# Kernel tuning notes

Measured on AMD Instinct MI355X. Metric: run time of the kernel, lower is better.

## Reference

```python
import jax, jax.numpy as jnp
import numpy as np

B, C, H, W = 64, 256, 64, 64
RATIO, K = 16, 8
PLANES = C // 2          # context_modeling hidden = int(in_planes*0.5)
HIDDEN = C // RATIO      # net hidden
ATT_CH = K // 2          # kernel-attention hidden
TEMP = 30.0
EPS = 1e-5


def setup_inputs() -> dict:
    key = jax.random.key(0)
    ks = jax.random.split(key, 16)
    s = lambda k, shape: jax.random.normal(k, shape, dtype=jnp.float32) * 0.05
    return {
        "x": jax.random.normal(ks[0], (B, C, H, W), dtype=jnp.float32),
        # conv_mask: Conv2d(C,1,1) with bias
        "w_mask": s(ks[1], (1, C)), "b_mask": jnp.zeros((1,), jnp.float32),
        # context_modeling: Conv2d(C,PLANES,1)+bias, LayerNorm([PLANES,1,1]), GELU, Conv2d(PLANES,C,1)+bias
        "w_cm1": s(ks[2], (PLANES, C)), "b_cm1": jnp.zeros((PLANES,), jnp.float32),
        "ln_w": jnp.ones((PLANES,), jnp.float32), "ln_b": jnp.zeros((PLANES,), jnp.float32),
        "w_cm2": s(ks[3], (C, PLANES)), "b_cm2": jnp.zeros((C,), jnp.float32),
        # net: Conv2d(C,HIDDEN,1,bias=False), ReLU, Conv2d(HIDDEN,K,1,bias=False)
        "w_net1": s(ks[4], (HIDDEN, C)), "w_net2": s(ks[5], (K, HIDDEN)),
        # kernel attention branch (K != 1)
        "w_fc": s(ks[6], (ATT_CH, K)),
        "bn_w": jnp.ones((ATT_CH,), jnp.float32), "bn_b": jnp.zeros((ATT_CH,), jnp.float32),
        "bn_mean": jnp.zeros((ATT_CH,), jnp.float32), "bn_var": jnp.ones((ATT_CH,), jnp.float32),
        "w_kfc": s(ks[7], (K, ATT_CH)),
    }


def reference(x, w_mask, b_mask, w_cm1, b_cm1, ln_w, ln_b, w_cm2, b_cm2,
              w_net1, w_net2, w_fc, bn_w, bn_b, bn_mean, bn_var, w_kfc):
    b, c, h, w = x.shape
    # beta_c: global average pool -> [B, C]
    beta_c = jnp.mean(x, axis=(2, 3))
    # global_pool: softmax(conv_mask(x)) over HW, spatially weighted sum of x
    mask = jnp.einsum('bchw,oc->bohw', x, w_mask)[:, 0] + b_mask[0]      # [B,H,W]
    mask = jax.nn.softmax(mask.reshape(b, h * w), axis=-1)               # softmax over HW
    context = jnp.einsum('bchw,bs->bc', x, mask.reshape(b, h, w).reshape(b, -1).reshape(b, h * w)) if False else \
        jnp.einsum('bcs,bs->bc', x.reshape(b, c, h * w), mask)           # [B,C]
    # context_modeling: 1x1 conv -> LayerNorm over channels -> GELU -> 1x1 conv
    t = context @ w_cm1.T + b_cm1                                        # [B, PLANES]
    mu = jnp.mean(t, axis=-1, keepdims=True)
    var = jnp.mean((t - mu) ** 2, axis=-1, keepdims=True)
    t = (t - mu) * jax.lax.rsqrt(var + EPS) * ln_w + ln_b
    t = jax.nn.gelu(t, approximate=False)
    beta_g = t @ w_cm2.T + b_cm2                                         # [B, C]
    # beta_s: channel-mean/max maps, tiled [avg,max,avg,max,...], spatial mean
    a = jnp.mean(jnp.mean(x, axis=1), axis=(1, 2))                       # [B]
    m = jnp.mean(jnp.max(x, axis=1), axis=(1, 2))                        # [B]
    beta_s = jnp.tile(jnp.stack([a, m], axis=-1), (1, c // 2))           # [B, C]
    out = beta_c + beta_g + beta_s                                       # [B, C]
    # net: conv1x1 -> ReLU -> conv1x1
    out = jax.nn.relu(out @ w_net1.T) @ w_net2.T                         # [B, K]
    # dynamic kernel attention (eval-mode BatchNorm on 1x1 spatial)
    ka = out @ w_fc.T                                                    # [B, K/2]
    ka = (ka - bn_mean) * jax.lax.rsqrt(bn_var + EPS) * bn_w + bn_b
    kernel = jax.nn.sigmoid(jax.nn.relu(ka) @ w_kfc.T)                   # [B, K]
    out = out * kernel
    return jax.nn.softmax(out / TEMP, axis=-1)                           # [B, K]
```

## Files before the change

kernel.cpp:

```cpp
#include <hip/hip_runtime.h>
#include <math.h>

#define BB   64
#define CC   256
#define HWQ  4096
#define TILE 64
#define ITER 8
#define QB   8
#define NBLK (BB * QB)
#define TPB  256

#define WS_BETA 0
#define WS_CTX  (NBLK * CC)
#define WS_Z    (2 * NBLK * CC)
#define WS_M    (WS_Z + NBLK)

__global__ __launch_bounds__(TPB, 2) void pass1(
    const float* __restrict__ x,
    const float* __restrict__ w_mask,
    const float* __restrict__ b_mask,
    float* __restrict__ ws)
{
    __shared__ __align__(16) float wm[CC];
    __shared__ __align__(16) float redL[1024];
    __shared__ __align__(16) float redM[1024];
    __shared__ __align__(16) float tileP[TILE];
    __shared__ __align__(16) float scrA[CC * 16];
    __shared__ __align__(16) float scrB[CC * 16];

    const int tid = threadIdx.x;
    const int b   = blockIdx.x >> 3;
    const int q   = blockIdx.x & 7;
    const int hi  = tid >> 4;
    const int j   = tid & 15;
    const float* xb = x + (size_t)b * CC * HWQ + q * (TILE * ITER);

    wm[tid] = w_mask[tid];

    float4 cur[16], nxt[16];
    #pragma unroll
    for (int i = 0; i < 16; ++i) {
        const int c = i * 16 + hi;
        cur[i] = *reinterpret_cast<const float4*>(xb + (size_t)c * HWQ + 4 * j);
    }
    __syncthreads();
    const float bm = b_mask[0];

    float smP[16], cxP[16];
    #pragma unroll
    for (int i = 0; i < 16; ++i) { smP[i] = 0.f; cxP[i] = 0.f; }
    float zTot = 0.f, mTot = 0.f;

    for (int it = 0; it < ITER; ++it) {
        float lp0 = 0.f, lp1 = 0.f, lp2 = 0.f, lp3 = 0.f;
        float mp0 = -3.4e38f, mp1 = -3.4e38f, mp2 = -3.4e38f, mp3 = -3.4e38f;
        #pragma unroll
        for (int i = 0; i < 16; ++i) {
            const float w = wm[i * 16 + hi];
            const float4 v = cur[i];
            lp0 = fmaf(w, v.x, lp0); lp1 = fmaf(w, v.y, lp1);
            lp2 = fmaf(w, v.z, lp2); lp3 = fmaf(w, v.w, lp3);
            mp0 = fmaxf(mp0, v.x); mp1 = fmaxf(mp1, v.y);
            mp2 = fmaxf(mp2, v.z); mp3 = fmaxf(mp3, v.w);
        }
        reinterpret_cast<float4*>(redL)[tid] = make_float4(lp0, lp1, lp2, lp3);
        reinterpret_cast<float4*>(redM)[tid] = make_float4(mp0, mp1, mp2, mp3);
        __syncthreads();

        if (tid < TILE) {
            float lg = 0.f, cm = -3.4e38f;
            #pragma unroll
            for (int h = 0; h < 16; ++h) {
                lg += redL[h * 64 + tid];
                cm = fmaxf(cm, redM[h * 64 + tid]);
            }
            const float p = expf(lg + bm);
            tileP[tid] = p;
            float zs = p, cs = cm;
            #pragma unroll
            for (int off = 32; off > 0; off >>= 1) {
                zs += __shfl_down(zs, off, 64);
                cs += __shfl_down(cs, off, 64);
            }
            if (tid == 0) { zTot += zs; mTot += cs; }
        }
        __syncthreads();

        if (it + 1 < ITER) {
            #pragma unroll
            for (int i = 0; i < 16; ++i) {
                const int c = i * 16 + hi;
                nxt[i] = *reinterpret_cast<const float4*>(
                    xb + (size_t)c * HWQ + (it + 1) * TILE + 4 * j);
            }
        }

        const float4 pv = reinterpret_cast<const float4*>(tileP)[j];
        #pragma unroll
        for (int i = 0; i < 16; ++i) {
            const float4 v = cur[i];
            smP[i] += (v.x + v.y) + (v.z + v.w);
            cxP[i] = fmaf(v.x, pv.x, fmaf(v.y, pv.y,
                     fmaf(v.z, pv.z, fmaf(v.w, pv.w, cxP[i]))));
        }
        if (it + 1 < ITER) {
            #pragma unroll
            for (int i = 0; i < 16; ++i) cur[i] = nxt[i];
        }
    }

    #pragma unroll
    for (int i = 0; i < 16; ++i) {
        scrA[(i * 16 + hi) * 16 + j] = smP[i];
        scrB[(i * 16 + hi) * 16 + j] = cxP[i];
    }
    __syncthreads();
    {
        const int c = tid;
        const float4* a4 = reinterpret_cast<const float4*>(&scrA[c * 16]);
        const float4* b4 = reinterpret_cast<const float4*>(&scrB[c * 16]);
        float sm = 0.f, cx = 0.f;
        #pragma unroll
        for (int g = 0; g < 4; ++g) {
            const float4 av = a4[g], bv = b4[g];
            sm += (av.x + av.y) + (av.z + av.w);
            cx += (bv.x + bv.y) + (bv.z + bv.w);
        }
        ws[WS_BETA + blockIdx.x * CC + c] = sm;
        ws[WS_CTX  + blockIdx.x * CC + c] = cx;
    }
    if (tid == 0) {
        ws[WS_Z + blockIdx.x] = zTot;
        ws[WS_M + blockIdx.x] = mTot;
    }
}

__global__ __launch_bounds__(TPB) void finalize(
    const float* __restrict__ ws,
    const float* __restrict__ w_cm1,  const float* __restrict__ b_cm1,
    const float* __restrict__ ln_w,   const float* __restrict__ ln_b,
    const float* __restrict__ w_cm2,  const float* __restrict__ b_cm2,
    const float* __restrict__ w_net1, const float* __restrict__ w_net2,
    const float* __restrict__ w_fc,   const float* __restrict__ bn_w,
    const float* __restrict__ bn_b,   const float* __restrict__ bn_mean,
    const float* __restrict__ bn_var, const float* __restrict__ w_kfc,
    float* __restrict__ out)
{
    __shared__ __align__(16) float s_beta[CC];
    __shared__ __align__(16) float s_ctx[CC];
    __shared__ __align__(16) float s_t[128];
    __shared__ __align__(16) float s_out[CC];
    __shared__ float s_h[16];
    __shared__ float s_o2[8];
    __shared__ float s_red[4];
    __shared__ float s_scal[4];
    __shared__ float s_zm[2];

    const int b = blockIdx.x, tid = threadIdx.x;

    float bc_s = 0.f, cx_s = 0.f;
    #pragma unroll
    for (int qq = 0; qq < QB; ++qq) {
        bc_s += ws[WS_BETA + (b * QB + qq) * CC + tid];
        cx_s += ws[WS_CTX  + (b * QB + qq) * CC + tid];
    }
    if (tid < 16) {
        float v = (tid < 8) ? ws[WS_Z + b * QB + tid] : ws[WS_M + b * QB + (tid - 8)];
        v += __shfl_down(v, 4, 64);
        v += __shfl_down(v, 2, 64);
        v += __shfl_down(v, 1, 64);
        if (tid == 0) s_zm[0] = v;
        if (tid == 8) s_zm[1] = v;
    }
    __syncthreads();

    const float bc = bc_s * (1.f / 4096.f);
    const float cx = cx_s / s_zm[0];
    s_beta[tid] = bc;
    s_ctx[tid]  = cx;

    float av = bc;
    #pragma unroll
    for (int off = 32; off > 0; off >>= 1) av += __shfl_down(av, off, 64);
    if ((tid & 63) == 0) s_red[tid >> 6] = av;
    __syncthreads();
    if (tid == 0) {
        s_scal[0] = (s_red[0] + s_red[1] + s_red[2] + s_red[3]) * (1.f / 256.f);
        s_scal[1] = s_zm[1] * (1.f / 4096.f);
    }
    __syncthreads();

    if (tid < 128) {
        const float4* wr = reinterpret_cast<const float4*>(w_cm1 + tid * 256);
        const float4* cr = reinterpret_cast<const float4*>(s_ctx);
        float acc = 0.f;
        #pragma unroll 4
        for (int i = 0; i < 64; ++i) {
            const float4 w = wr[i], c4 = cr[i];
            acc = fmaf(w.x, c4.x, acc); acc = fmaf(w.y, c4.y, acc);
            acc = fmaf(w.z, c4.z, acc); acc = fmaf(w.w, c4.w, acc);
        }
        s_t[tid] = acc + b_cm1[tid];
    }
    __syncthreads();

    if (tid < 64) {
        float v = s_t[tid] + s_t[tid + 64];
        #pragma unroll
        for (int off = 32; off > 0; off >>= 1) v += __shfl_down(v, off, 64);
        float mu = __shfl(v, 0, 64) * (1.f / 128.f);
        const float d0 = s_t[tid] - mu, d1 = s_t[tid + 64] - mu;
        float vv = d0 * d0 + d1 * d1;
        #pragma unroll
        for (int off = 32; off > 0; off >>= 1) vv += __shfl_down(vv, off, 64);
        if (tid == 0) {
            s_scal[2] = mu;
            s_scal[3] = rsqrtf(vv * (1.f / 128.f) + 1e-5f);
        }
    }
    __syncthreads();

    if (tid < 128) {
        float g = (s_t[tid] - s_scal[2]) * s_scal[3] * ln_w[tid] + ln_b[tid];
        g = 0.5f * g * (1.0f + erff(g * 0.70710678118654752f));
        s_t[tid] = g;
    }
    __syncthreads();

    {
        const float4* wr = reinterpret_cast<const float4*>(w_cm2 + tid * 128);
        const float4* gr = reinterpret_cast<const float4*>(s_t);
        float acc = 0.f;
        #pragma unroll 4
        for (int i = 0; i < 32; ++i) {
            const float4 w = wr[i], g = gr[i];
            acc = fmaf(w.x, g.x, acc); acc = fmaf(w.y, g.y, acc);
            acc = fmaf(w.z, g.z, acc); acc = fmaf(w.w, g.w, acc);
        }
        const float bs = (tid & 1) ? s_scal[1] : s_scal[0];
        s_out[tid] = s_beta[tid] + acc + b_cm2[tid] + bs;
    }
    __syncthreads();

    if (tid < 16) {
        const float4* wr = reinterpret_cast<const float4*>(w_net1 + tid * 256);
        const float4* orr = reinterpret_cast<const float4*>(s_out);
        float acc = 0.f;
        #pragma unroll 4
        for (int i = 0; i < 64; ++i) {
            const float4 w = wr[i], o = orr[i];
            acc = fmaf(w.x, o.x, acc); acc = fmaf(w.y, o.y, acc);
            acc = fmaf(w.z, o.z, acc); acc = fmaf(w.w, o.w, acc);
        }
        s_h[tid] = fmaxf(acc, 0.f);
    }
    __syncthreads();

    if (tid < 8) {
        float acc = 0.f;
        #pragma unroll
        for (int jj = 0; jj < 16; ++jj) acc += s_h[jj] * w_net2[tid * 16 + jj];
        s_o2[tid] = acc;
    }
    __syncthreads();

    if (tid == 0) {
        float r[4];
        #pragma unroll
        for (int p = 0; p < 4; ++p) {
            float acc = 0.f;
            #pragma unroll
            for (int k = 0; k < 8; ++k) acc += s_o2[k] * w_fc[p * 8 + k];
            acc = (acc - bn_mean[p]) * rsqrtf(bn_var[p] + 1e-5f) * bn_w[p] + bn_b[p];
            r[p] = fmaxf(acc, 0.f);
        }
        float v[8], vmax = -3.4e38f;
        #pragma unroll
        for (int k = 0; k < 8; ++k) {
            float acc = 0.f;
            #pragma unroll
            for (int p = 0; p < 4; ++p) acc += r[p] * w_kfc[k * 4 + p];
            const float kr = 1.f / (1.f + expf(-acc));
            v[k] = s_o2[k] * kr * (1.f / 30.f);
            vmax = fmaxf(vmax, v[k]);
        }
        float zs = 0.f;
        #pragma unroll
        for (int k = 0; k < 8; ++k) { v[k] = expf(v[k] - vmax); zs += v[k]; }
        const float inv = 1.f / zs;
        #pragma unroll
        for (int k = 0; k < 8; ++k) out[b * 8 + k] = v[k] * inv;
    }
}

extern "C" void kernel_launch(void* const* d_in, const int* in_sizes, int n_in,
                              void* d_out, int out_size, void* d_ws, size_t ws_size,
                              hipStream_t stream) {
    const float* x       = (const float*)d_in[0];
    const float* w_mask  = (const float*)d_in[1];
    const float* b_mask  = (const float*)d_in[2];
    const float* w_cm1   = (const float*)d_in[3];
    const float* b_cm1   = (const float*)d_in[4];
    const float* ln_w    = (const float*)d_in[5];
    const float* ln_b    = (const float*)d_in[6];
    const float* w_cm2   = (const float*)d_in[7];
    const float* b_cm2   = (const float*)d_in[8];
    const float* w_net1  = (const float*)d_in[9];
    const float* w_net2  = (const float*)d_in[10];
    const float* w_fc    = (const float*)d_in[11];
    const float* bn_w    = (const float*)d_in[12];
    const float* bn_b    = (const float*)d_in[13];
    const float* bn_mean = (const float*)d_in[14];
    const float* bn_var  = (const float*)d_in[15];
    const float* w_kfc   = (const float*)d_in[16];
    float* out = (float*)d_out;
    float* ws  = (float*)d_ws;

    pass1<<<NBLK, TPB, 0, stream>>>(x, w_mask, b_mask, ws);
    finalize<<<BB, TPB, 0, stream>>>(ws, w_cm1, b_cm1, ln_w, ln_b, w_cm2, b_cm2,
                                     w_net1, w_net2, w_fc, bn_w, bn_b, bn_mean,
                                     bn_var, w_kfc, out);
}
```

Before: 410.8 us.

## Split pass1 into more blocks, drop register prefetch, shrink LDS for occupancy

```diff
diff --git a/kernel.cpp b/kernel.cpp
--- a/kernel.cpp
+++ b/kernel.cpp
@@ -5,8 +5,8 @@
 #define CC   256
 #define HWQ  4096
 #define TILE 64
-#define ITER 8
-#define QB   8
+#define ITER 4
+#define QB   16
 #define NBLK (BB * QB)
 #define TPB  256
 
@@ -15,34 +15,26 @@
 #define WS_Z    (2 * NBLK * CC)
 #define WS_M    (WS_Z + NBLK)
 
-__global__ __launch_bounds__(TPB, 2) void pass1(
+__global__ __launch_bounds__(TPB, 4) void pass1(
     const float* __restrict__ x,
     const float* __restrict__ w_mask,
     const float* __restrict__ b_mask,
     float* __restrict__ ws)
 {
     __shared__ __align__(16) float wm[CC];
-    __shared__ __align__(16) float redL[1024];
-    __shared__ __align__(16) float redM[1024];
+    __shared__ __align__(16) float redL[16 * 64];
+    __shared__ __align__(16) float redM[16 * 64];
     __shared__ __align__(16) float tileP[TILE];
-    __shared__ __align__(16) float scrA[CC * 16];
-    __shared__ __align__(16) float scrB[CC * 16];
+    __shared__ float scr[CC * 17];
 
     const int tid = threadIdx.x;
-    const int b   = blockIdx.x >> 3;
-    const int q   = blockIdx.x & 7;
+    const int b   = blockIdx.x >> 4;
+    const int q   = blockIdx.x & 15;
     const int hi  = tid >> 4;
     const int j   = tid & 15;
     const float* xb = x + (size_t)b * CC * HWQ + q * (TILE * ITER);
 
     wm[tid] = w_mask[tid];
-
-    float4 cur[16], nxt[16];
-    #pragma unroll
-    for (int i = 0; i < 16; ++i) {
-        const int c = i * 16 + hi;
-        cur[i] = *reinterpret_cast<const float4*>(xb + (size_t)c * HWQ + 4 * j);
-    }
     __syncthreads();
     const float bm = b_mask[0];
 
@@ -52,6 +44,14 @@
     float zTot = 0.f, mTot = 0.f;
 
     for (int it = 0; it < ITER; ++it) {
+        float4 cur[16];
+        #pragma unroll
+        for (int i = 0; i < 16; ++i) {
+            const int c = i * 16 + hi;
+            cur[i] = *reinterpret_cast<const float4*>(
+                xb + (size_t)c * HWQ + it * TILE + 4 * j);
+        }
+
         float lp0 = 0.f, lp1 = 0.f, lp2 = 0.f, lp3 = 0.f;
         float mp0 = -3.4e38f, mp1 = -3.4e38f, mp2 = -3.4e38f, mp3 = -3.4e38f;
         #pragma unroll
@@ -68,32 +68,26 @@
         __syncthreads();
 
         if (tid < TILE) {
-            float lg = 0.f, cm = -3.4e38f;
-            #pragma unroll
-            for (int h = 0; h < 16; ++h) {
-                lg += redL[h * 64 + tid];
-                cm = fmaxf(cm, redM[h * 64 + tid]);
-            }
+            float lg = 0.f;
+            #pragma unroll
+            for (int h = 0; h < 16; ++h) lg += redL[h * 64 + tid];
             const float p = expf(lg + bm);
             tileP[tid] = p;
-            float zs = p, cs = cm;
-            #pragma unroll
-            for (int off = 32; off > 0; off >>= 1) {
-                zs += __shfl_down(zs, off, 64);
-                cs += __shfl_down(cs, off, 64);
-            }
-            if (tid == 0) { zTot += zs; mTot += cs; }
+            float zs = p;
+            #pragma unroll
+            for (int off = 32; off > 0; off >>= 1) zs += __shfl_down(zs, off, 64);
+            if (tid == 0) zTot += zs;
+        } else if (tid < 2 * TILE) {
+            const int s = tid - TILE;
+            float cm = -3.4e38f;
+            #pragma unroll
+            for (int h = 0; h < 16; ++h) cm = fmaxf(cm, redM[h * 64 + s]);
+            float cs = cm;
+            #pragma unroll
+            for (int off = 32; off > 0; off >>= 1) cs += __shfl_down(cs, off, 64);
+            if (tid == TILE) mTot += cs;
         }
         __syncthreads();
-
-        if (it + 1 < ITER) {
-            #pragma unroll
-            for (int i = 0; i < 16; ++i) {
-                const int c = i * 16 + hi;
-                nxt[i] = *reinterpret_cast<const float4*>(
-                    xb + (size_t)c * HWQ + (it + 1) * TILE + 4 * j);
-            }
-        }
 
         const float4 pv = reinterpret_cast<const float4*>(tileP)[j];
         #pragma unroll
@@ -103,36 +97,29 @@
             cxP[i] = fmaf(v.x, pv.x, fmaf(v.y, pv.y,
                      fmaf(v.z, pv.z, fmaf(v.w, pv.w, cxP[i]))));
         }
-        if (it + 1 < ITER) {
-            #pragma unroll
-            for (int i = 0; i < 16; ++i) cur[i] = nxt[i];
-        }
-    }
-
-    #pragma unroll
-    for (int i = 0; i < 16; ++i) {
-        scrA[(i * 16 + hi) * 16 + j] = smP[i];
-        scrB[(i * 16 + hi) * 16 + j] = cxP[i];
-    }
+    }
+
+    #pragma unroll
+    for (int i = 0; i < 16; ++i) scr[(i * 16 + hi) * 17 + j] = smP[i];
     __syncthreads();
     {
-        const int c = tid;
-        const float4* a4 = reinterpret_cast<const float4*>(&scrA[c * 16]);
-        const float4* b4 = reinterpret_cast<const float4*>(&scrB[c * 16]);
-        float sm = 0.f, cx = 0.f;
-        #pragma unroll
-        for (int g = 0; g < 4; ++g) {
-            const float4 av = a4[g], bv = b4[g];
-            sm += (av.x + av.y) + (av.z + av.w);
-            cx += (bv.x + bv.y) + (bv.z + bv.w);
-        }
-        ws[WS_BETA + blockIdx.x * CC + c] = sm;
-        ws[WS_CTX  + blockIdx.x * CC + c] = cx;
-    }
-    if (tid == 0) {
-        ws[WS_Z + blockIdx.x] = zTot;
-        ws[WS_M + blockIdx.x] = mTot;
-    }
+        float sm = 0.f;
+        #pragma unroll
+        for (int k = 0; k < 16; ++k) sm += scr[tid * 17 + k];
+        ws[WS_BETA + blockIdx.x * CC + tid] = sm;
+    }
+    __syncthreads();
+    #pragma unroll
+    for (int i = 0; i < 16; ++i) scr[(i * 16 + hi) * 17 + j] = cxP[i];
+    __syncthreads();
+    {
+        float cx = 0.f;
+        #pragma unroll
+        for (int k = 0; k < 16; ++k) cx += scr[tid * 17 + k];
+        ws[WS_CTX + blockIdx.x * CC + tid] = cx;
+    }
+    if (tid == 0)    ws[WS_Z + blockIdx.x] = zTot;
+    if (tid == TILE) ws[WS_M + blockIdx.x] = mTot;
 }
 
 __global__ __launch_bounds__(TPB) void finalize(
@@ -164,13 +151,15 @@
         bc_s += ws[WS_BETA + (b * QB + qq) * CC + tid];
         cx_s += ws[WS_CTX  + (b * QB + qq) * CC + tid];
     }
-    if (tid < 16) {
-        float v = (tid < 8) ? ws[WS_Z + b * QB + tid] : ws[WS_M + b * QB + (tid - 8)];
+    if (tid < 32) {
+        float v = (tid < 16) ? ws[WS_Z + b * QB + tid]
+                             : ws[WS_M + b * QB + (tid - 16)];
+        v += __shfl_down(v, 8, 64);
         v += __shfl_down(v, 4, 64);
         v += __shfl_down(v, 2, 64);
         v += __shfl_down(v, 1, 64);
-        if (tid == 0) s_zm[0] = v;
-        if (tid == 8) s_zm[1] = v;
+        if (tid == 0)  s_zm[0] = v;
+        if (tid == 16) s_zm[1] = v;
     }
     __syncthreads();
 
```

New measurement: 420.2 us. +2.3%, slower.
